# Kernel optimization log

Hardware: AMD Instinct MI355X
Metric: run time of the kernel (lower is better)

## Reference

```python
import jax, jax.numpy as jnp
import numpy as np

N_ANCH = 100800   # 3 * (160^2 + 80^2 + 40^2), YOLOv5 @ 1280
NUM_CLS = 80
IMG_HW = 1280
MAX_DETS = 300    # fixed padding for jit-compatible NMS output
OUT = 224
SCORE_THRESH = 0.1
IOU_THRESH = 0.45
ALLOWED = jnp.array([1, 2, 3, 4, 6, 8, 17, 18, 44], dtype=jnp.int32)
MEAN = jnp.array([0.485, 0.456, 0.406], dtype=jnp.float32).reshape(1, 3, 1, 1)
STD = jnp.array([0.229, 0.224, 0.225], dtype=jnp.float32).reshape(1, 3, 1, 1)


def setup_inputs() -> dict:
    key = jax.random.key(0)
    k1, k2, k3, k4, k5 = jax.random.split(key, 5)
    # realistic YOLO-style raw predictions: cx,cy in-image, modest w,h, gaussian class logits
    cxcy = jax.random.uniform(k1, (1, 2, N_ANCH), dtype=jnp.float32) * IMG_HW
    wh = jax.random.uniform(k2, (1, 2, N_ANCH), dtype=jnp.float32) * 256.0 + 8.0
    obj = jax.random.uniform(k3, (1, 1, N_ANCH), dtype=jnp.float32)
    logits = jax.random.normal(k4, (1, NUM_CLS, N_ANCH), dtype=jnp.float32)
    raw_pred = jnp.concatenate([cxcy, wh, obj, logits], axis=1)  # [1, 5+C, N]
    image = jax.random.uniform(k5, (1, 3, IMG_HW, IMG_HW), dtype=jnp.float32)
    return {"raw_pred": raw_pred, "image": image}


def _pairwise_iou(b):
    # b: [K,4] xyxy
    area = (b[:, 2] - b[:, 0]) * (b[:, 3] - b[:, 1])
    lt = jnp.maximum(b[:, None, :2], b[None, :, :2])
    rb = jnp.minimum(b[:, None, 2:], b[None, :, 2:])
    wh = jnp.clip(rb - lt, 0.0)
    inter = wh[..., 0] * wh[..., 1]
    union = area[:, None] + area[None, :] - inter
    return inter / jnp.maximum(union, 1e-9)


def _nms_keep(iou, valid):
    # greedy NMS over score-sorted boxes; returns boolean keep mask [K]
    K = iou.shape[0]
    idx = jnp.arange(K)

    def body(i, keep):
        suppress = keep[i] & (iou[i] > IOU_THRESH) & (idx > i)
        return keep & ~suppress

    return jax.lax.fori_loop(0, K, body, valid)


def _roi_align(image_chw, boxes):
    # torchvision roi_align, aligned=True, one sample per bin at the bin center
    # (sampling_ratio fixed to 1; see notes). image_chw: [3,H,W], boxes: [M,4]
    C, H, W = image_chw.shape
    grid = (jnp.arange(OUT, dtype=jnp.float32) + 0.5) / OUT  # fractional bin centers

    def one(box):
        x1, y1, x2, y2 = box
        xs = x1 - 0.5 + grid * (x2 - x1)  # [OUT], aligned=True half-pixel offset
        ys = y1 - 0.5 + grid * (y2 - y1)
        vx = (xs >= -1.0) & (xs <= W)
        vy = (ys >= -1.0) & (ys <= H)
        xc = jnp.clip(xs, 0.0, W - 1)
        yc = jnp.clip(ys, 0.0, H - 1)
        x0 = jnp.floor(xc).astype(jnp.int32)
        y0 = jnp.floor(yc).astype(jnp.int32)
        x1i = jnp.minimum(x0 + 1, W - 1)
        y1i = jnp.minimum(y0 + 1, H - 1)
        lx = xc - x0
        ly = yc - y0
        # bilinear gather: [3, OUT, OUT]
        v00 = image_chw[:, y0[:, None], x0[None, :]]
        v01 = image_chw[:, y0[:, None], x1i[None, :]]
        v10 = image_chw[:, y1i[:, None], x0[None, :]]
        v11 = image_chw[:, y1i[:, None], x1i[None, :]]
        top = v00 * (1.0 - lx) + v01 * lx
        bot = v10 * (1.0 - lx) + v11 * lx
        val = top * (1.0 - ly)[None, :, None] + bot * ly[None, :, None]
        return jnp.where(vy[None, :, None] & vx[None, None, :], val, 0.0)

    return jax.vmap(one)(boxes)


def _forward(raw_pred, image):
    x = raw_pred[0].T  # [N, 5+C]
    cx, cy, w, h = x[:, 0], x[:, 1], x[:, 2], x[:, 3]
    boxes = jnp.stack([cx - w / 2, cy - h / 2, cx + w / 2, cy + h / 2], axis=1)
    cls_logits = x[:, 5:]
    scores = cls_logits.max(axis=1)
    classes = cls_logits.argmax(axis=1).astype(jnp.int32) + 1
    # score + allowed-class filter (mask form)
    mask = (scores > SCORE_THRESH) & jnp.isin(classes, ALLOWED)
    masked_scores = jnp.where(mask, scores, jnp.finfo(scores.dtype).min)
    top_scores, top_idx = jax.lax.top_k(masked_scores, MAX_DETS)  # sorted desc
    top_boxes = boxes[top_idx]
    top_classes = classes[top_idx]
    valid = mask[top_idx]
    # greedy NMS over padded top-K candidates
    keep = _nms_keep(_pairwise_iou(top_boxes), valid)
    final_boxes = jnp.where(keep[:, None], top_boxes, 0.0)
    final_scores = jnp.where(keep, top_scores, 0.0)
    final_classes = jnp.where(keep, top_classes, 0)
    # crops: full image first, then RoIAlign crops, normalized once
    full_crop = jax.image.resize(image, (1, 3, OUT, OUT), method='linear', antialias=False)
    roi_crops = _roi_align(image[0], final_boxes)  # [K,3,224,224]
    roi_crops = jnp.where(keep[:, None, None, None], roi_crops, 0.0)
    all_crops = jnp.concatenate([full_crop, roi_crops], axis=0)  # [K+1,3,224,224]
    all_crops = (all_crops - MEAN) / STD
    return final_boxes, final_scores, final_classes, all_crops, keep


def reference(raw_pred, image):
    return _forward(raw_pred, image)
```

## Files before the change

kernel.cpp:

```cpp
#include <hip/hip_runtime.h>
#include <stdint.h>

#define N_ANCH   100800
#define NUM_CLS  80
#define IMG_HW   1280
#define MAX_DETS 300
#define OUTSZ    224
#define CAND_CAP 4096

#define OFF_BOXES   0
#define OFF_SCORES  1200
#define OFF_CLASSES 1500
#define OFF_CROPS   1800
#define CROPS_ELEMS (301 * 3 * 224 * 224)
#define OFF_KEEP    (OFF_CROPS + CROPS_ELEMS)

#define SC_HIST   0
#define SC_CNT    262144
#define SC_THRESH 262148
#define SC_CAND   262208
#define SC_KEYS   294976
#define SC_CLS    698176

__device__ __forceinline__ uint32_t fkey(float f) {
    uint32_t u = __float_as_uint(f);
    return (u & 0x80000000u) ? ~u : (u | 0x80000000u);
}
__device__ __forceinline__ float unfkey(uint32_t k) {
    uint32_t u = (k & 0x80000000u) ? (k & 0x7fffffffu) : ~k;
    return __uint_as_float(u);
}

__global__ void k_score(const float* __restrict__ rp, uint32_t* __restrict__ keys,
                        uint32_t* __restrict__ hist, uint32_t* __restrict__ clsarr) {
    int a = blockIdx.x * 256 + threadIdx.x;
    if (a >= N_ANCH) return;
    float best = -3.402823466e38f;
    int bi = 0;
    for (int c = 0; c < NUM_CLS; ++c) {
        float v = rp[(5 + c) * N_ANCH + a];
        if (v > best) { best = v; bi = c; }
    }
    int cls = bi + 1;
    clsarr[a] = (uint32_t)cls;
    const unsigned long long AM =
        (1ULL << 1) | (1ULL << 2) | (1ULL << 3) | (1ULL << 4) | (1ULL << 6) |
        (1ULL << 8) | (1ULL << 17) | (1ULL << 18) | (1ULL << 44);
    bool m = (best > 0.1f) && (cls < 64) && ((AM >> cls) & 1ULL);
    uint32_t key = m ? fkey(best) : 0u;
    keys[a] = key;
    if (m) atomicAdd(&hist[key >> 16], 1u);
}

__global__ void k_scan(const uint32_t* __restrict__ hist, uint32_t* __restrict__ thresh_out) {
    __shared__ uint32_t seg[256];
    int t = threadIdx.x;
    uint32_t s = 0;
    for (int k = 0; k < 256; ++k) s += hist[t * 256 + k];
    seg[t] = s;
    __syncthreads();
    if (t == 0) {
        uint32_t acc = 0;
        int bin = 0, sIdx = -1;
        for (int i = 255; i >= 0; --i) {
            if (acc + seg[i] >= (uint32_t)MAX_DETS) { sIdx = i; break; }
            acc += seg[i];
        }
        if (sIdx >= 0) {
            for (int b = sIdx * 256 + 255; b >= sIdx * 256; --b) {
                acc += hist[b];
                if (acc >= (uint32_t)MAX_DETS) { bin = b; break; }
            }
        }
        *thresh_out = (uint32_t)bin;
    }
}

__global__ void k_compact(const uint32_t* __restrict__ keys, const uint32_t* __restrict__ thresh_p,
                          unsigned long long* __restrict__ cand, uint32_t* __restrict__ cnt) {
    int a = blockIdx.x * 256 + threadIdx.x;
    if (a >= N_ANCH) return;
    uint32_t key = keys[a];
    uint32_t tb = *thresh_p;
    if (key != 0u && (key >> 16) >= tb) {
        uint32_t pos = atomicAdd(cnt, 1u);
        if (pos < CAND_CAP)
            cand[pos] = ((unsigned long long)key << 32) | (uint32_t)(~(uint32_t)a);
    }
}

__global__ void __launch_bounds__(1024) k_select(const float* __restrict__ rp,
                                                 const uint32_t* __restrict__ clsarr,
                                                 const unsigned long long* __restrict__ cand,
                                                 const uint32_t* __restrict__ cnt_p,
                                                 float* __restrict__ out) {
    __shared__ unsigned long long sb[CAND_CAP];
    __shared__ float sbx[MAX_DETS][4];
    __shared__ float sscore[MAX_DETS];
    __shared__ int   scls[MAX_DETS];
    __shared__ __align__(8) uint32_t sup[MAX_DETS][10];
    __shared__ __align__(8) uint32_t kw[10];
    __shared__ __align__(8) uint32_t rnz[10];
    int t = threadIdx.x;
    int n = min((int)(*cnt_p), CAND_CAP);

    int S = 1024;
    while (S < n) S <<= 1;

    for (int i = t; i < S; i += 1024) sb[i] = (i < n) ? cand[i] : 0ull;
    __syncthreads();

    for (int k = 2; k <= S; k <<= 1) {
        for (int j = k >> 1; j > 0; j >>= 1) {
            for (int i = t; i < S; i += 1024) {
                int l = i ^ j;
                if (l > i) {
                    unsigned long long a = sb[i], b = sb[l];
                    bool up = ((i & k) == 0);
                    if ((up && a < b) || (!up && a > b)) { sb[i] = b; sb[l] = a; }
                }
            }
            __syncthreads();
        }
    }

    for (int i = t; i < MAX_DETS * 10; i += 1024) ((uint32_t*)sup)[i] = 0u;
    if (t < 10) { kw[t] = 0u; rnz[t] = 0u; }
    __syncthreads();

    if (t < MAX_DETS) {
        unsigned long long key = sb[t];
        bool valid = (t < n) && (key != 0ull);
        float score = 0.f; int cls = 0;
        float b0 = 0.f, b1 = 0.f, b2 = 0.f, b3 = 0.f;
        if (valid) {
            uint32_t a = ~(uint32_t)(key & 0xffffffffull);
            score = unfkey((uint32_t)(key >> 32));
            float cx = rp[a], cy = rp[N_ANCH + a];
            float w = rp[2 * N_ANCH + a], h = rp[3 * N_ANCH + a];
            b0 = cx - w * 0.5f; b1 = cy - h * 0.5f;
            b2 = cx + w * 0.5f; b3 = cy + h * 0.5f;
            cls = (int)clsarr[a];
            atomicOr(&kw[t >> 5], 1u << (t & 31));
        }
        sbx[t][0] = b0; sbx[t][1] = b1; sbx[t][2] = b2; sbx[t][3] = b3;
        sscore[t] = score; scls[t] = cls;
    }
    __syncthreads();

    for (int p = t; p < MAX_DETS * MAX_DETS; p += 1024) {
        int i = p / MAX_DETS, j = p % MAX_DETS;
        if (j > i) {
            float ax1 = sbx[i][0], ay1 = sbx[i][1], ax2 = sbx[i][2], ay2 = sbx[i][3];
            float bx1 = sbx[j][0], by1 = sbx[j][1], bx2 = sbx[j][2], by2 = sbx[j][3];
            float areaA = (ax2 - ax1) * (ay2 - ay1);
            float areaB = (bx2 - bx1) * (by2 - by1);
            float ltx = fmaxf(ax1, bx1), lty = fmaxf(ay1, by1);
            float rbx = fminf(ax2, bx2), rby = fminf(ay2, by2);
            float iw = fmaxf(rbx - ltx, 0.f), ih = fmaxf(rby - lty, 0.f);
            float inter = iw * ih;
            float uni = areaA + areaB - inter;
            float iou = inter / fmaxf(uni, 1e-9f);
            if (iou > 0.45f) {
                atomicOr(&sup[i][j >> 5], 1u << (j & 31));
                atomicOr(&rnz[i >> 5], 1u << (i & 31));
            }
        }
    }
    __syncthreads();

    if (t == 0) {
        unsigned long long kwr[5], rnzr[5];
        const unsigned long long* kq = (const unsigned long long*)kw;
        const unsigned long long* rq = (const unsigned long long*)rnz;
        #pragma unroll
        for (int w = 0; w < 5; ++w) { kwr[w] = kq[w]; rnzr[w] = rq[w]; }
        #pragma unroll
        for (int s = 0; s < 5; ++s) {
            int lim = (s == 4) ? (MAX_DETS - 4 * 64) : 64;
            for (int i2 = 0; i2 < lim; ++i2) {
                if (((kwr[s] >> i2) & 1ull) && ((rnzr[s] >> i2) & 1ull)) {
                    int i = s * 64 + i2;
                    const unsigned long long* row = (const unsigned long long*)&sup[i][0];
                    unsigned long long r0 = row[0], r1 = row[1], r2 = row[2],
                                       r3 = row[3], r4 = row[4];
                    kwr[0] &= ~r0; kwr[1] &= ~r1; kwr[2] &= ~r2;
                    kwr[3] &= ~r3; kwr[4] &= ~r4;
                }
            }
        }
        unsigned long long* kqo = (unsigned long long*)kw;
        #pragma unroll
        for (int w = 0; w < 5; ++w) kqo[w] = kwr[w];
    }
    __syncthreads();

    if (t < MAX_DETS) {
        bool kp = (kw[t >> 5] >> (t & 31)) & 1u;
        out[OFF_BOXES + t * 4 + 0] = kp ? sbx[t][0] : 0.f;
        out[OFF_BOXES + t * 4 + 1] = kp ? sbx[t][1] : 0.f;
        out[OFF_BOXES + t * 4 + 2] = kp ? sbx[t][2] : 0.f;
        out[OFF_BOXES + t * 4 + 3] = kp ? sbx[t][3] : 0.f;
        out[OFF_SCORES + t]  = kp ? sscore[t] : 0.f;
        out[OFF_CLASSES + t] = kp ? (float)scls[t] : 0.f;
        out[OFF_KEEP + t]    = kp ? 1.f : 0.f;
    }
}

__device__ __forceinline__ float bilerp(const float* __restrict__ ch, float xc, float yc) {
    int x0 = (int)floorf(xc), y0 = (int)floorf(yc);
    int x1 = min(x0 + 1, IMG_HW - 1), y1 = min(y0 + 1, IMG_HW - 1);
    float lx = xc - (float)x0, ly = yc - (float)y0;
    float v00 = ch[y0 * IMG_HW + x0], v01 = ch[y0 * IMG_HW + x1];
    float v10 = ch[y1 * IMG_HW + x0], v11 = ch[y1 * IMG_HW + x1];
    return (v00 * (1.f - lx) + v01 * lx) * (1.f - ly) +
           (v10 * (1.f - lx) + v11 * lx) * ly;
}

__global__ void k_crops(const float* __restrict__ img, float* __restrict__ out) {
    int nc = blockIdx.y;
    int n = nc / 3, c = nc % 3;
    int q = blockIdx.x * 256 + threadIdx.x;
    int oy = q / (OUTSZ / 4);
    int ox0 = (q % (OUTSZ / 4)) * 4;
    const float meanv[3] = {0.485f, 0.456f, 0.406f};
    const float stdv[3]  = {0.229f, 0.224f, 0.225f};
    float mean = meanv[c], rstd = 1.0f / stdv[c];
    const float* ch = img + c * IMG_HW * IMG_HW;
    float4 v;
    if (n == 0) {
        float sy = ((float)oy + 0.5f) * (1280.0f / 224.0f) - 0.5f;
        float r[4];
        #pragma unroll
        for (int k = 0; k < 4; ++k) {
            float sx = ((float)(ox0 + k) + 0.5f) * (1280.0f / 224.0f) - 0.5f;
            r[k] = (bilerp(ch, sx, sy) - mean) * rstd;
        }
        v = make_float4(r[0], r[1], r[2], r[3]);
    } else {
        float kp = out[OFF_KEEP + (n - 1)];
        if (kp == 0.f) {
            float z = (0.f - mean) * rstd;
            v = make_float4(z, z, z, z);
        } else {
            float x1b = out[OFF_BOXES + (n - 1) * 4 + 0];
            float y1b = out[OFF_BOXES + (n - 1) * 4 + 1];
            float x2b = out[OFF_BOXES + (n - 1) * 4 + 2];
            float y2b = out[OFF_BOXES + (n - 1) * 4 + 3];
            float gy = ((float)oy + 0.5f) / 224.0f;
            float ys = y1b - 0.5f + gy * (y2b - y1b);
            bool vy = (ys >= -1.0f) && (ys <= 1280.0f);
            float yc = fminf(fmaxf(ys, 0.f), 1279.f);
            float r[4];
            #pragma unroll
            for (int k = 0; k < 4; ++k) {
                float gx = ((float)(ox0 + k) + 0.5f) / 224.0f;
                float xs = x1b - 0.5f + gx * (x2b - x1b);
                bool vx = (xs >= -1.0f) && (xs <= 1280.0f);
                float xc = fminf(fmaxf(xs, 0.f), 1279.f);
                float val = bilerp(ch, xc, yc);
                if (!(vx && vy)) val = 0.f;
                r[k] = (val - mean) * rstd;
            }
            v = make_float4(r[0], r[1], r[2], r[3]);
        }
    }
    *(float4*)(out + OFF_CROPS + (size_t)nc * (OUTSZ * OUTSZ) + oy * OUTSZ + ox0) = v;
}

extern "C" void kernel_launch(void* const* d_in, const int* in_sizes, int n_in,
                              void* d_out, int out_size, void* d_ws, size_t ws_size,
                              hipStream_t stream) {
    (void)in_sizes; (void)n_in; (void)out_size; (void)d_ws; (void)ws_size;
    const float* rp  = (const float*)d_in[0];
    const float* img = (const float*)d_in[1];
    float* out = (float*)d_out;
    char* sbase = (char*)d_out + (size_t)OFF_CROPS * sizeof(float);
    uint32_t* hist = (uint32_t*)(sbase + SC_HIST);
    uint32_t* cnt  = (uint32_t*)(sbase + SC_CNT);
    uint32_t* thr  = (uint32_t*)(sbase + SC_THRESH);
    unsigned long long* cand = (unsigned long long*)(sbase + SC_CAND);
    uint32_t* keys = (uint32_t*)(sbase + SC_KEYS);
    uint32_t* clsa = (uint32_t*)(sbase + SC_CLS);

    hipMemsetAsync(sbase, 0, SC_CAND, stream);
    k_score<<<(N_ANCH + 255) / 256, 256, 0, stream>>>(rp, keys, hist, clsa);
    k_scan<<<1, 256, 0, stream>>>(hist, thr);
    k_compact<<<(N_ANCH + 255) / 256, 256, 0, stream>>>(keys, thr, cand, cnt);
    k_select<<<1, 1024, 0, stream>>>(rp, clsa, cand, cnt, out);
    dim3 grid(49, 903);
    k_crops<<<grid, 256, 0, stream>>>(img, out);
}
```

Baseline: 378.2 us.

## Vectorize score/compact loads, replace bitonic sort with rank select, nontemporal crop stores

The score and compact kernels now each handle four anchors per thread with float4/uint4 loads and stores, which cuts the thread count and the number of memory instructions. The single-block bitonic sort over up to 4096 candidates is replaced by a counting-rank selection that writes the top 300 keys straight into place. The O(n^2) rank loop costs more when the candidate count is large, but it removes the many barrier stages of the sort. Crop outputs are now written with nontemporal vector stores, meant to avoid polluting the cache with about 180 MB of write-once data.

```diff
diff --git a/kernel.cpp b/kernel.cpp
--- a/kernel.cpp
+++ b/kernel.cpp
@@ -22,6 +22,8 @@
 #define SC_KEYS   294976
 #define SC_CLS    698176
 
+typedef float f32x4 __attribute__((ext_vector_type(4)));
+
 __device__ __forceinline__ uint32_t fkey(float f) {
     uint32_t u = __float_as_uint(f);
     return (u & 0x80000000u) ? ~u : (u | 0x80000000u);
@@ -33,23 +35,33 @@
 
 __global__ void k_score(const float* __restrict__ rp, uint32_t* __restrict__ keys,
                         uint32_t* __restrict__ hist, uint32_t* __restrict__ clsarr) {
-    int a = blockIdx.x * 256 + threadIdx.x;
-    if (a >= N_ANCH) return;
-    float best = -3.402823466e38f;
-    int bi = 0;
+    int a4 = (blockIdx.x * 256 + threadIdx.x) * 4;
+    if (a4 >= N_ANCH) return;
+    float best[4] = {-3.402823466e38f, -3.402823466e38f, -3.402823466e38f, -3.402823466e38f};
+    int bi[4] = {0, 0, 0, 0};
     for (int c = 0; c < NUM_CLS; ++c) {
-        float v = rp[(5 + c) * N_ANCH + a];
-        if (v > best) { best = v; bi = c; }
-    }
-    int cls = bi + 1;
-    clsarr[a] = (uint32_t)cls;
+        float4 v = *(const float4*)&rp[(5 + c) * N_ANCH + a4];
+        if (v.x > best[0]) { best[0] = v.x; bi[0] = c; }
+        if (v.y > best[1]) { best[1] = v.y; bi[1] = c; }
+        if (v.z > best[2]) { best[2] = v.z; bi[2] = c; }
+        if (v.w > best[3]) { best[3] = v.w; bi[3] = c; }
+    }
     const unsigned long long AM =
         (1ULL << 1) | (1ULL << 2) | (1ULL << 3) | (1ULL << 4) | (1ULL << 6) |
         (1ULL << 8) | (1ULL << 17) | (1ULL << 18) | (1ULL << 44);
-    bool m = (best > 0.1f) && (cls < 64) && ((AM >> cls) & 1ULL);
-    uint32_t key = m ? fkey(best) : 0u;
-    keys[a] = key;
-    if (m) atomicAdd(&hist[key >> 16], 1u);
+    uint32_t kv[4], cv[4];
+    #pragma unroll
+    for (int k = 0; k < 4; ++k) {
+        int cls = bi[k] + 1;
+        cv[k] = (uint32_t)cls;
+        bool m = (best[k] > 0.1f) && (cls < 64) && ((AM >> cls) & 1ULL);
+        kv[k] = m ? fkey(best[k]) : 0u;
+    }
+    *(uint4*)&keys[a4]   = make_uint4(kv[0], kv[1], kv[2], kv[3]);
+    *(uint4*)&clsarr[a4] = make_uint4(cv[0], cv[1], cv[2], cv[3]);
+    #pragma unroll
+    for (int k = 0; k < 4; ++k)
+        if (kv[k]) atomicAdd(&hist[kv[k] >> 16], 1u);
 }
 
 __global__ void k_scan(const uint32_t* __restrict__ hist, uint32_t* __restrict__ thresh_out) {
@@ -78,14 +90,21 @@
 
 __global__ void k_compact(const uint32_t* __restrict__ keys, const uint32_t* __restrict__ thresh_p,
                           unsigned long long* __restrict__ cand, uint32_t* __restrict__ cnt) {
-    int a = blockIdx.x * 256 + threadIdx.x;
-    if (a >= N_ANCH) return;
-    uint32_t key = keys[a];
+    int a4 = (blockIdx.x * 256 + threadIdx.x) * 4;
+    if (a4 >= N_ANCH) return;
+    uint4 kv = *(const uint4*)&keys[a4];
     uint32_t tb = *thresh_p;
-    if (key != 0u && (key >> 16) >= tb) {
-        uint32_t pos = atomicAdd(cnt, 1u);
-        if (pos < CAND_CAP)
-            cand[pos] = ((unsigned long long)key << 32) | (uint32_t)(~(uint32_t)a);
+    uint32_t ks[4] = {kv.x, kv.y, kv.z, kv.w};
+    #pragma unroll
+    for (int k = 0; k < 4; ++k) {
+        uint32_t key = ks[k];
+        if (key != 0u && (key >> 16) >= tb) {
+            uint32_t pos = atomicAdd(cnt, 1u);
+            if (pos < CAND_CAP) {
+                uint32_t a = (uint32_t)(a4 + k);
+                cand[pos] = ((unsigned long long)key << 32) | (uint32_t)(~a);
+            }
+        }
     }
 }
 
@@ -95,6 +114,7 @@
                                                  const uint32_t* __restrict__ cnt_p,
                                                  float* __restrict__ out) {
     __shared__ unsigned long long sb[CAND_CAP];
+    __shared__ unsigned long long top[MAX_DETS];
     __shared__ float sbx[MAX_DETS][4];
     __shared__ float sscore[MAX_DETS];
     __shared__ int   scls[MAX_DETS];
@@ -104,33 +124,25 @@
     int t = threadIdx.x;
     int n = min((int)(*cnt_p), CAND_CAP);
 
-    int S = 1024;
-    while (S < n) S <<= 1;
-
-    for (int i = t; i < S; i += 1024) sb[i] = (i < n) ? cand[i] : 0ull;
-    __syncthreads();
-
-    for (int k = 2; k <= S; k <<= 1) {
-        for (int j = k >> 1; j > 0; j >>= 1) {
-            for (int i = t; i < S; i += 1024) {
-                int l = i ^ j;
-                if (l > i) {
-                    unsigned long long a = sb[i], b = sb[l];
-                    bool up = ((i & k) == 0);
-                    if ((up && a < b) || (!up && a > b)) { sb[i] = b; sb[l] = a; }
-                }
-            }
-            __syncthreads();
-        }
-    }
+    for (int i = t; i < n; i += 1024) sb[i] = cand[i];
+    if (t < MAX_DETS) top[t] = 0ull;
+    __syncthreads();
+
+    for (int i = t; i < n; i += 1024) {
+        unsigned long long key = sb[i];
+        int rank = 0;
+        for (int j = 0; j < n; ++j) rank += (sb[j] > key) ? 1 : 0;
+        if (rank < MAX_DETS) top[rank] = key;
+    }
+    __syncthreads();
 
     for (int i = t; i < MAX_DETS * 10; i += 1024) ((uint32_t*)sup)[i] = 0u;
     if (t < 10) { kw[t] = 0u; rnz[t] = 0u; }
     __syncthreads();
 
     if (t < MAX_DETS) {
-        unsigned long long key = sb[t];
-        bool valid = (t < n) && (key != 0ull);
+        unsigned long long key = top[t];
+        bool valid = (key != 0ull);
         float score = 0.f; int cls = 0;
         float b0 = 0.f, b1 = 0.f, b2 = 0.f, b3 = 0.f;
         if (valid) {
@@ -227,21 +239,19 @@
     const float stdv[3]  = {0.229f, 0.224f, 0.225f};
     float mean = meanv[c], rstd = 1.0f / stdv[c];
     const float* ch = img + c * IMG_HW * IMG_HW;
-    float4 v;
+    f32x4 v;
     if (n == 0) {
         float sy = ((float)oy + 0.5f) * (1280.0f / 224.0f) - 0.5f;
-        float r[4];
         #pragma unroll
         for (int k = 0; k < 4; ++k) {
             float sx = ((float)(ox0 + k) + 0.5f) * (1280.0f / 224.0f) - 0.5f;
-            r[k] = (bilerp(ch, sx, sy) - mean) * rstd;
-        }
-        v = make_float4(r[0], r[1], r[2], r[3]);
+            v[k] = (bilerp(ch, sx, sy) - mean) * rstd;
+        }
     } else {
         float kp = out[OFF_KEEP + (n - 1)];
         if (kp == 0.f) {
             float z = (0.f - mean) * rstd;
-            v = make_float4(z, z, z, z);
+            v = (f32x4){z, z, z, z};
         } else {
             float x1b = out[OFF_BOXES + (n - 1) * 4 + 0];
             float y1b = out[OFF_BOXES + (n - 1) * 4 + 1];
@@ -251,7 +261,6 @@
             float ys = y1b - 0.5f + gy * (y2b - y1b);
             bool vy = (ys >= -1.0f) && (ys <= 1280.0f);
             float yc = fminf(fmaxf(ys, 0.f), 1279.f);
-            float r[4];
             #pragma unroll
             for (int k = 0; k < 4; ++k) {
                 float gx = ((float)(ox0 + k) + 0.5f) / 224.0f;
@@ -260,12 +269,12 @@
                 float xc = fminf(fmaxf(xs, 0.f), 1279.f);
                 float val = bilerp(ch, xc, yc);
                 if (!(vx && vy)) val = 0.f;
-                r[k] = (val - mean) * rstd;
-            }
-            v = make_float4(r[0], r[1], r[2], r[3]);
-        }
-    }
-    *(float4*)(out + OFF_CROPS + (size_t)nc * (OUTSZ * OUTSZ) + oy * OUTSZ + ox0) = v;
+                v[k] = (val - mean) * rstd;
+            }
+        }
+    }
+    f32x4* dst = (f32x4*)(out + OFF_CROPS + (size_t)nc * (OUTSZ * OUTSZ) + oy * OUTSZ + ox0);
+    __builtin_nontemporal_store(v, dst);
 }
 
 extern "C" void kernel_launch(void* const* d_in, const int* in_sizes, int n_in,
@@ -284,9 +293,9 @@
     uint32_t* clsa = (uint32_t*)(sbase + SC_CLS);
 
     hipMemsetAsync(sbase, 0, SC_CAND, stream);
-    k_score<<<(N_ANCH + 255) / 256, 256, 0, stream>>>(rp, keys, hist, clsa);
+    k_score<<<(N_ANCH / 4 + 255) / 256, 256, 0, stream>>>(rp, keys, hist, clsa);
     k_scan<<<1, 256, 0, stream>>>(hist, thr);
-    k_compact<<<(N_ANCH + 255) / 256, 256, 0, stream>>>(keys, thr, cand, cnt);
+    k_compact<<<(N_ANCH / 4 + 255) / 256, 256, 0, stream>>>(keys, thr, cand, cnt);
     k_select<<<1, 1024, 0, stream>>>(rp, clsa, cand, cnt, out);
     dim3 grid(49, 903);
     k_crops<<<grid, 256, 0, stream>>>(img, out);
```

Measured after the change: 371.1 us. Within noise of the previous version (-1.9%).
